# Performance work log

Measured on AMD Instinct MI355X. Metric: run time of the kernel, lower is better.

## Reference

```python
import jax, jax.numpy as jnp
import numpy as np

B, N, C, H = 4, 4096, 128, 4


def setup_inputs() -> dict:
    key = jax.random.key(0)
    ks = jax.random.split(key, 12)
    def rn(k, shape, s=0.02):
        return jax.random.normal(k, shape, jnp.float32) * s
    return dict(
        x=jax.random.normal(ks[0], (B, N, C), jnp.float32),
        p=jax.random.normal(ks[1], (B, N, 3), jnp.float32),
        fcl1_w=rn(ks[2], (C, C)), fcl1_b=jnp.zeros((C,), jnp.float32),
        # per-head (stacked over leading H axis) TransformerLayer params
        hq_w=rn(ks[3], (H, C, C)), hq_b=jnp.zeros((H, C), jnp.float32),
        hk_w=rn(ks[4], (H, C, C)), hk_b=jnp.zeros((H, C), jnp.float32),
        hv_w=rn(ks[5], (H, C, C)), hv_b=jnp.zeros((H, C), jnp.float32),
        pe1_w=rn(ks[6], (H, C, 3)), pe1_b=jnp.zeros((H, C), jnp.float32),  # Conv1d(3->C, k=1)
        pe2_w=rn(ks[7], (H, C, C)), pe2_b=jnp.zeros((H, C), jnp.float32),  # Conv1d(C->C, k=1)
        mh_w=rn(ks[8], (C, 4 * C)), mh_b=jnp.zeros((C,), jnp.float32),
        fcl2_w=rn(ks[9], (C, C)), fcl2_b=jnp.zeros((C,), jnp.float32),
    )


def reference(x, p, fcl1_w, fcl1_b, hq_w, hq_b, hk_w, hk_b, hv_w, hv_b,
              pe1_w, pe1_b, pe2_w, pe2_b, mh_w, mh_b, fcl2_w, fcl2_b):
    residual = x
    xf = x @ fcl1_w.T + fcl1_b  # fcl1
    scale = 1.0 / jnp.sqrt(jnp.asarray(C, jnp.float32))

    def head(qw, qb, kw, kb, vw, vb, p1w, p1b, p2w, p2b):
        # kernel-size-1 Conv1d == pointwise linear over coords
        pe = jax.nn.relu(jnp.einsum('bnd,cd->bnc', p, p1w) + p1b)
        pe = jnp.einsum('bnc,dc->bnd', pe, p2w) + p2b
        xh = xf + pe
        q = xh @ kw.T + kb  # note: original uses self.key for x_query
        k = xh @ qw.T + qb  # and self.query for x_key (name swap, kept faithful)
        v = xh @ vw.T + vb
        s = jax.nn.softmax(jnp.einsum('bnc,bmc->bnm', q, k) * scale, axis=-1)
        return jnp.einsum('bnm,bmc->bnc', s, v)

    outs = jax.vmap(head)(hq_w, hq_b, hk_w, hk_b, hv_w, hv_b,
                          pe1_w, pe1_b, pe2_w, pe2_b)  # [H,B,N,C]
    cat = jnp.moveaxis(outs, 0, 2).reshape(B, N, H * C)  # concat head1..head4 on last dim
    y = cat @ mh_w.T + mh_b
    y = y @ fcl2_w.T + fcl2_b
    mu = jnp.mean(y, axis=-1, keepdims=True)
    var = jnp.var(y, axis=-1, keepdims=True)
    y = (y - mu) / jnp.sqrt(var + 1e-5)  # torch.layer_norm, no affine
    return (y + residual, p)
```

## Files before the change

kernel.cpp:

```cpp
#include <hip/hip_runtime.h>
#include <hip/hip_bf16.h>

typedef __bf16 bf16;
typedef bf16 bf16x8 __attribute__((ext_vector_type(8)));
typedef float f32x4 __attribute__((ext_vector_type(4)));

static __device__ __forceinline__ f32x4 mfma16(bf16x8 a, bf16x8 b, f32x4 c) {
  return __builtin_amdgcn_mfma_f32_16x16x32_bf16(a, b, c, 0, 0, 0);
}

typedef __attribute__((address_space(3))) void lds_t;
typedef const __attribute__((address_space(1))) void gm_t;

#define N_SEG 18
#define TOTAL_CONV 2511616

__global__ void probe_k(const unsigned short* __restrict__ xr, int* __restrict__ flag) {
  int wild = 0;
#pragma unroll
  for (int i = 0; i < 8; i++) {
    unsigned short w = xr[threadIdx.x * 8 + i];
    int e = (w >> 7) & 0xFF;
    if (e < 110 || e > 134) wild++;
  }
#pragma unroll
  for (int off = 1; off < 64; off <<= 1) wild += __shfl_xor(wild, off);
  if (threadIdx.x == 0) *flag = (wild > 64) ? 1 : 0;
}

struct ConvArgs { const void* src[N_SEG]; };

__global__ __launch_bounds__(256) void convall_k(ConvArgs a, bf16* __restrict__ dst,
                                                 void* __restrict__ outp,
                                                 const int* __restrict__ flag) {
  const int ends[N_SEG] = {2097152, 2146304, 2162688, 2162816, 2228352, 2228864,
                           2294400, 2294912, 2360448, 2360960, 2362496, 2363008,
                           2428544, 2429056, 2494592, 2495104, 2511488, 2511616};
  int i = blockIdx.x * 256 + threadIdx.x;
  if (i >= TOTAL_CONV) {
    int j = i - TOTAL_CONV;
    if (j < 49152) {
      if (*flag) ((float*)outp)[2097152 + j] = ((const float*)a.src[1])[j];
      else       ((bf16*)outp)[2097152 + j]  = ((const bf16*)a.src[1])[j];
    }
    return;
  }
  int s = 0;
  while (i >= ends[s]) s++;
  int j = i - (s ? ends[s - 1] : 0);
  if (*flag) dst[i] = (bf16)((const float*)a.src[s])[j];
  else       dst[i] = ((const bf16*)a.src[s])[j];
}

__global__ __launch_bounds__(256, 2) void pre_k(
    const bf16* __restrict__ x, const bf16* __restrict__ p,
    const bf16* __restrict__ f1w, const bf16* __restrict__ f1b,
    const bf16* __restrict__ pe1w, const bf16* __restrict__ pe1b,
    const bf16* __restrict__ pe2w, const bf16* __restrict__ pe2b,
    const bf16* __restrict__ Wq, const bf16* __restrict__ Bq,
    const bf16* __restrict__ Wk, const bf16* __restrict__ Bk,
    const bf16* __restrict__ Wv, const bf16* __restrict__ Bv,
    bf16* __restrict__ qo, bf16* __restrict__ ko, bf16* __restrict__ vo)
{
  const int lane = threadIdx.x & 63;
  const int wave = threadIdx.x >> 6;
  const int quad = lane >> 4;
  const int n15 = lane & 15;
  const int h = blockIdx.y;
  const int r0 = blockIdx.x * 64;
  const int wr = wave * 16;

  __shared__ bf16 tile[9216];

  f32x4 acc[8];
  const f32x4 zz = {};

  {
    bf16x8 ap = {};
    if (quad == 0) {
      const bf16* pr = p + (long)(r0 + wr + n15) * 3;
      ap[0] = pr[0]; ap[1] = pr[1]; ap[2] = pr[2];
    }
#pragma unroll
    for (int ct = 0; ct < 8; ct++) {
      bf16x8 bw = {};
      if (quad == 0) {
        const bf16* wp = pe1w + ((long)h * 128 + ct * 16 + n15) * 3;
        bw[0] = wp[0]; bw[1] = wp[1]; bw[2] = wp[2];
      }
      acc[ct] = mfma16(ap, bw, zz);
    }
#pragma unroll
    for (int ct = 0; ct < 8; ct++) {
      const int col = ct * 16 + n15;
      const float bb = (float)pe1b[h * 128 + col];
#pragma unroll
      for (int r = 0; r < 4; r++)
        tile[(wr + quad * 4 + r) * 136 + col] = (bf16)fmaxf(acc[ct][r] + bb, 0.f);
    }
  }

#pragma unroll
  for (int ct = 0; ct < 8; ct++) acc[ct] = zz;
#pragma unroll
  for (int kk = 0; kk < 4; kk++) {
    const int ka = kk * 32 + quad * 8;
    bf16x8 a0 = *(const bf16x8*)&tile[(wr + n15) * 136 + ka];
#pragma unroll
    for (int ct = 0; ct < 8; ct++) {
      bf16x8 wf = *(const bf16x8*)(pe2w + (long)h * 16384 + (long)(ct * 16 + n15) * 128 + ka);
      acc[ct] = mfma16(a0, wf, acc[ct]);
    }
  }
#pragma unroll
  for (int kk = 0; kk < 4; kk++) {
    const int ka = kk * 32 + quad * 8;
    bf16x8 a0 = *(const bf16x8*)(x + (long)(r0 + wr + n15) * 128 + ka);
#pragma unroll
    for (int ct = 0; ct < 8; ct++) {
      bf16x8 wf = *(const bf16x8*)(f1w + (long)(ct * 16 + n15) * 128 + ka);
      acc[ct] = mfma16(a0, wf, acc[ct]);
    }
  }
#pragma unroll
  for (int ct = 0; ct < 8; ct++) {
    const int col = ct * 16 + n15;
    const float bv = (float)pe2b[h * 128 + col] + (float)f1b[col];
#pragma unroll
    for (int r = 0; r < 4; r++)
      tile[(wr + quad * 4 + r) * 136 + col] = (bf16)(acc[ct][r] + bv);
  }

  bf16x8 af[4];
#pragma unroll
  for (int kk = 0; kk < 4; kk++)
    af[kk] = *(const bf16x8*)&tile[(wr + n15) * 136 + kk * 32 + quad * 8];

#pragma unroll
  for (int m = 0; m < 2; m++) {
    f32x4 a2[8];
#pragma unroll
    for (int ct = 0; ct < 8; ct++) a2[ct] = zz;
    const bf16* Wm = (m == 0) ? Wq : Wk;
#pragma unroll
    for (int kk = 0; kk < 4; kk++) {
      const int ka = kk * 32 + quad * 8;
#pragma unroll
      for (int ct = 0; ct < 8; ct++) {
        bf16x8 wf = *(const bf16x8*)(Wm + (long)h * 16384 + (long)(ct * 16 + n15) * 128 + ka);
        a2[ct] = mfma16(af[kk], wf, a2[ct]);
      }
    }
    bf16* oz = ((m == 0) ? qo : ko) + (long)h * 2097152;
    const bf16* Bz = (m == 0) ? Bq : Bk;
    const float sc = (m == 0) ? 0.12751743f : 1.0f;
#pragma unroll
    for (int ct = 0; ct < 8; ct++) {
      const int col = ct * 16 + n15;
      const float bv = (float)Bz[h * 128 + col];
#pragma unroll
      for (int r = 0; r < 4; r++)
        oz[(long)(r0 + wr + quad * 4 + r) * 128 + col] = (bf16)((a2[ct][r] + bv) * sc);
    }
  }

  {
    f32x4 a2[8];
#pragma unroll
    for (int ct = 0; ct < 8; ct++) a2[ct] = zz;
#pragma unroll
    for (int kk = 0; kk < 4; kk++) {
      const int ka = kk * 32 + quad * 8;
#pragma unroll
      for (int ct = 0; ct < 8; ct++) {
        bf16x8 wf = *(const bf16x8*)(Wv + (long)h * 16384 + (long)(ct * 16 + n15) * 128 + ka);
        a2[ct] = mfma16(af[kk], wf, a2[ct]);
      }
    }
    __syncthreads();
#pragma unroll
    for (int ct = 0; ct < 8; ct++) {
      const int col = ct * 16 + n15;
      const float bv = (float)Bv[h * 128 + col];
#pragma unroll
      for (int r = 0; r < 4; r++)
        tile[col * 72 + (wr + quad * 4 + r)] = (bf16)(a2[ct][r] + bv);
    }
    __syncthreads();
    bf16* vz = vo + (long)h * 2097152;
#pragma unroll
    for (int i = 0; i < 16; i++) {
      const int c = wave * 32 + i * 2 + (lane >> 5);
      const int m2 = (lane & 31) * 2;
      *(unsigned int*)&vz[(long)c * 16384 + r0 + m2] =
          *(const unsigned int*)&tile[c * 72 + m2];
    }
  }
}

__global__ __launch_bounds__(256, 2) void attn_k(
    const bf16* __restrict__ Q, const bf16* __restrict__ Kg,
    const bf16* __restrict__ vT, bf16* __restrict__ Op, float* __restrict__ ls)
{
  const int lane = threadIdx.x & 63;
  const int wave = threadIdx.x >> 6;
  const int quad = lane >> 4;
  const int n15 = lane & 15;
  const int qt = blockIdx.x >> 1;
  const int half = blockIdx.x & 1;
  const int b = blockIdx.y, h = blockIdx.z;
  const long qkBase = ((long)h * 4 + b) * 4096 * 128;
  const long vBase = (long)h * (128L * 16384) + (long)b * 4096;
  const int wrow = qt * 128 + wave * 32;
  const int kvStart = half * 2048;

  __shared__ bf16 Kt[2][64 * 128];
  __shared__ bf16 Vt[2][128 * 64];
  __shared__ bf16 Pt[8][1024];

  bf16x8 qf[2][4];
#pragma unroll
  for (int g = 0; g < 2; g++)
#pragma unroll
    for (int kk = 0; kk < 4; kk++)
      qf[g][kk] = *(const bf16x8*)(Q + qkBase + (long)(wrow + g * 16 + n15) * 128 + kk * 32 + quad * 8);

  const int krl  = lane >> 4;
  const int kpch = lane & 15;
  const int vcl  = lane >> 3;
  const int vpch = lane & 7;

  f32x4 Om[2][8] = {};
  float l_part[2][4] = {};

#pragma unroll
  for (int i = 0; i < 4; i++) {
    const int row = wave * 16 + i * 4 + krl;
    const int ch = kpch ^ (row & 15);
    __builtin_amdgcn_global_load_lds(
        (gm_t*)(Kg + qkBase + (long)(kvStart + row) * 128 + ch * 8),
        (lds_t*)&Kt[0][(wave * 16 + i * 4) * 128], 16, 0, 0);
  }
#pragma unroll
  for (int i = 0; i < 4; i++) {
    const int c = wave * 32 + i * 8 + vcl;
    const int vch = vpch ^ (c & 7);
    __builtin_amdgcn_global_load_lds(
        (gm_t*)(vT + vBase + (long)c * 16384 + kvStart + vch * 8),
        (lds_t*)&Vt[0][(wave * 32 + i * 8) * 64], 16, 0, 0);
  }

  for (int it = 0; it < 32; it++) {
    __syncthreads();
    const int cb = it & 1;
    if (it + 1 < 32) {
      const int kv1 = kvStart + (it + 1) * 64;
      const int nb = cb ^ 1;
#pragma unroll
      for (int i = 0; i < 4; i++) {
        const int row = wave * 16 + i * 4 + krl;
        const int ch = kpch ^ (row & 15);
        __builtin_amdgcn_global_load_lds(
            (gm_t*)(Kg + qkBase + (long)(kv1 + row) * 128 + ch * 8),
            (lds_t*)&Kt[nb][(wave * 16 + i * 4) * 128], 16, 0, 0);
      }
#pragma unroll
      for (int i = 0; i < 4; i++) {
        const int c = wave * 32 + i * 8 + vcl;
        const int vch = vpch ^ (c & 7);
        __builtin_amdgcn_global_load_lds(
            (gm_t*)(vT + vBase + (long)c * 16384 + kv1 + vch * 8),
            (lds_t*)&Vt[nb][(wave * 32 + i * 8) * 64], 16, 0, 0);
      }
    }

    f32x4 S[2][4] = {};
#pragma unroll
    for (int kk = 0; kk < 4; kk++) {
#pragma unroll
      for (int ct = 0; ct < 4; ct++) {
        bf16x8 kf = *(const bf16x8*)&Kt[cb][(ct * 16 + n15) * 128 + (((kk * 4 + quad) ^ n15) * 8)];
        S[0][ct] = mfma16(qf[0][kk], kf, S[0][ct]);
        S[1][ct] = mfma16(qf[1][kk], kf, S[1][ct]);
      }
    }

#pragma unroll
    for (int g = 0; g < 2; g++)
#pragma unroll
      for (int ct = 0; ct < 4; ct++)
#pragma unroll
        for (int r = 0; r < 4; r++) {
          float e = __builtin_amdgcn_exp2f(S[g][ct][r]);
          l_part[g][r] += e;
          const int row = quad * 4 + r;
          const int kv = ct * 16 + n15;
          Pt[wave * 2 + g][row * 64 + ((((kv >> 3) ^ (row & 7)) * 8)) + (kv & 7)] = (bf16)e;
        }

#pragma unroll
    for (int kk = 0; kk < 2; kk++) {
      bf16x8 vf[8];
#pragma unroll
      for (int ct = 0; ct < 8; ct++) {
        const int c = ct * 16 + n15;
        vf[ct] = *(const bf16x8*)&Vt[cb][c * 64 + (((kk * 4 + quad) ^ (c & 7)) * 8)];
      }
#pragma unroll
      for (int g = 0; g < 2; g++) {
        bf16x8 pf = *(const bf16x8*)&Pt[wave * 2 + g][n15 * 64 + (((kk * 4 + quad) ^ (n15 & 7)) * 8)];
#pragma unroll
        for (int ct = 0; ct < 8; ct++)
          Om[g][ct] = mfma16(pf, vf[ct], Om[g][ct]);
      }
    }
  }

#pragma unroll
  for (int g = 0; g < 2; g++) {
#pragma unroll
    for (int r = 0; r < 4; r++) {
      float s = l_part[g][r];
#pragma unroll
      for (int off = 1; off < 16; off <<= 1) s += __shfl_xor(s, off);
      if (n15 == 0)
        ls[((long)half * 4 + h) * 16384 + b * 4096 + wrow + g * 16 + quad * 4 + r] = s;
    }
    const long ob = (long)half * 8388608 + (long)(b * 4096 + wrow + g * 16 + quad * 4) * 512 + h * 128;
#pragma unroll
    for (int ct = 0; ct < 8; ct++)
#pragma unroll
      for (int r = 0; r < 4; r++)
        Op[ob + (long)r * 512 + ct * 16 + n15] = (bf16)Om[g][ct][r];
  }
}

__global__ __launch_bounds__(256) void tail_k(
    const bf16* __restrict__ Op, const float* __restrict__ ls,
    const bf16* __restrict__ mhw, const bf16* __restrict__ mhb,
    const bf16* __restrict__ f2w, const bf16* __restrict__ f2b,
    const void* __restrict__ xraw, void* __restrict__ outraw,
    const int* __restrict__ flag)
{
  const int lane = threadIdx.x & 63;
  const int wave = threadIdx.x >> 6;
  const int quad = lane >> 4;
  const int n15 = lane & 15;
  const int r0 = blockIdx.x * 64 + wave * 16;
  __shared__ bf16 y1t[64][136];

  float invA[4];
#pragma unroll
  for (int hh = 0; hh < 4; hh++) {
    const float l0 = ls[(long)hh * 16384 + r0 + n15];
    const float l1 = ls[(long)(4 + hh) * 16384 + r0 + n15];
    invA[hh] = 1.f / (l0 + l1);
  }

  f32x4 acc[8] = {};
  for (int k0 = 0; k0 < 512; k0 += 32) {
    const int hh = k0 >> 7;
    const int ka = k0 + quad * 8;
    bf16x8 v0 = *(const bf16x8*)(Op + (long)(r0 + n15) * 512 + ka);
    bf16x8 v1 = *(const bf16x8*)(Op + 8388608L + (long)(r0 + n15) * 512 + ka);
    bf16x8 a0;
#pragma unroll
    for (int j = 0; j < 8; j++)
      a0[j] = (bf16)(((float)v0[j] + (float)v1[j]) * invA[hh]);
#pragma unroll
    for (int ct = 0; ct < 8; ct++) {
      bf16x8 wf = *(const bf16x8*)(mhw + (long)(ct * 16 + n15) * 512 + ka);
      acc[ct] = mfma16(a0, wf, acc[ct]);
    }
  }
#pragma unroll
  for (int ct = 0; ct < 8; ct++) {
    const float bv = (float)mhb[ct * 16 + n15];
#pragma unroll
    for (int r = 0; r < 4; r++)
      y1t[wave * 16 + quad * 4 + r][ct * 16 + n15] = (bf16)(acc[ct][r] + bv);
  }

  f32x4 acc2[8] = {};
  for (int k0 = 0; k0 < 128; k0 += 32) {
    const int ka = k0 + quad * 8;
    bf16x8 a0 = *(const bf16x8*)&y1t[wave * 16 + n15][ka];
#pragma unroll
    for (int ct = 0; ct < 8; ct++) {
      bf16x8 wf = *(const bf16x8*)(f2w + (long)(ct * 16 + n15) * 128 + ka);
      acc2[ct] = mfma16(a0, wf, acc2[ct]);
    }
  }

  float s1[4] = {}, s2[4] = {};
#pragma unroll
  for (int ct = 0; ct < 8; ct++) {
    const float bv = (float)f2b[ct * 16 + n15];
#pragma unroll
    for (int r = 0; r < 4; r++) {
      const float v = acc2[ct][r] + bv;
      acc2[ct][r] = v;
      s1[r] += v;
      s2[r] += v * v;
    }
  }
  float mu[4], inv[4];
#pragma unroll
  for (int r = 0; r < 4; r++) {
    float a = s1[r], b2 = s2[r];
#pragma unroll
    for (int off = 1; off < 16; off <<= 1) {
      a += __shfl_xor(a, off);
      b2 += __shfl_xor(b2, off);
    }
    mu[r] = a * (1.f / 128.f);
    const float var = fmaxf(b2 * (1.f / 128.f) - mu[r] * mu[r], 0.f);
    inv[r] = rsqrtf(var + 1e-5f);
  }

  const int isF32 = *flag;
#pragma unroll
  for (int ct = 0; ct < 8; ct++)
#pragma unroll
    for (int r = 0; r < 4; r++) {
      const long idx = (long)(r0 + quad * 4 + r) * 128 + ct * 16 + n15;
      const float resid = isF32 ? ((const float*)xraw)[idx]
                                : (float)((const bf16*)xraw)[idx];
      const float v = (acc2[ct][r] - mu[r]) * inv[r] + resid;
      if (isF32) ((float*)outraw)[idx] = v;
      else       ((bf16*)outraw)[idx] = (bf16)v;
    }
}

extern "C" void kernel_launch(void* const* d_in, const int* in_sizes, int n_in,
                              void* d_out, int out_size, void* d_ws, size_t ws_size,
                              hipStream_t stream)
{
  bf16* ws  = (bf16*)d_ws;
  bf16* q   = ws;
  bf16* kb  = ws + 8388608;
  bf16* vt  = ws + 16777216;
  bf16* Op  = ws + 25165824;
  float* lsb = (float*)(ws + 41943040);
  const long AR = 42205184;
  int* flag = (int*)(ws + 44720000);

  static const int counts[N_SEG] = {2097152, 49152, 16384, 128, 65536, 512, 65536, 512,
                                    65536, 512, 1536, 512, 65536, 512, 65536, 512, 16384, 128};
  long offs[N_SEG]; long o = AR;
  for (int i = 0; i < N_SEG; i++) { offs[i] = o; o += counts[i]; }
  bf16* xc    = ws + offs[0];
  bf16* pc    = ws + offs[1];
  bf16* f1w   = ws + offs[2];
  bf16* f1b   = ws + offs[3];
  bf16* hqw   = ws + offs[4];
  bf16* hqb   = ws + offs[5];
  bf16* hkw   = ws + offs[6];
  bf16* hkb   = ws + offs[7];
  bf16* hvw   = ws + offs[8];
  bf16* hvb   = ws + offs[9];
  bf16* pe1w  = ws + offs[10];
  bf16* pe1b  = ws + offs[11];
  bf16* pe2w  = ws + offs[12];
  bf16* pe2b  = ws + offs[13];
  bf16* mhw   = ws + offs[14];
  bf16* mhb   = ws + offs[15];
  bf16* f2w   = ws + offs[16];
  bf16* f2b   = ws + offs[17];

  probe_k<<<dim3(1), dim3(64), 0, stream>>>((const unsigned short*)d_in[0], flag);
  ConvArgs ca;
  for (int i = 0; i < N_SEG; i++) ca.src[i] = d_in[i];
  convall_k<<<dim3((TOTAL_CONV + 49152 + 255) / 256), dim3(256), 0, stream>>>(ca, ws + AR, d_out, flag);

  dim3 blk(256);
  pre_k<<<dim3(256, 4), blk, 0, stream>>>(xc, pc, f1w, f1b, pe1w, pe1b, pe2w, pe2b,
                                          hkw, hkb, hqw, hqb, hvw, hvb, q, kb, vt);
  attn_k<<<dim3(64, 4, 4), blk, 0, stream>>>(q, kb, vt, Op, lsb);
  tail_k<<<dim3(256), blk, 0, stream>>>(Op, lsb, mhw, mhb, f2w, f2b, d_in[0], d_out, flag);
}
```

Before: 360.8 us.

## Drop KV split in attention, normalize in-kernel, fold dtype probe into conversion

The attention kernel no longer splits the key/value range into two halves. Each block now processes all 4096 keys and normalizes by the row sum before writing a single bf16 concat buffer. This removes the partial-output and row-sum buffers and the combine step in the tail kernel, at the cost of half as many attention blocks (512 instead of 1024) with twice the loop length. The separate dtype-probe launch is also merged into the conversion kernel: every block now recomputes the flag from the first 512 elements of x, which removes one launch.

```diff
diff --git a/kernel.cpp b/kernel.cpp
--- a/kernel.cpp
+++ b/kernel.cpp
@@ -15,32 +15,35 @@
 #define N_SEG 18
 #define TOTAL_CONV 2511616
 
-__global__ void probe_k(const unsigned short* __restrict__ xr, int* __restrict__ flag) {
-  int wild = 0;
-#pragma unroll
-  for (int i = 0; i < 8; i++) {
-    unsigned short w = xr[threadIdx.x * 8 + i];
-    int e = (w >> 7) & 0xFF;
-    if (e < 110 || e > 134) wild++;
-  }
-#pragma unroll
-  for (int off = 1; off < 64; off <<= 1) wild += __shfl_xor(wild, off);
-  if (threadIdx.x == 0) *flag = (wild > 64) ? 1 : 0;
-}
-
 struct ConvArgs { const void* src[N_SEG]; };
 
 __global__ __launch_bounds__(256) void convall_k(ConvArgs a, bf16* __restrict__ dst,
                                                  void* __restrict__ outp,
-                                                 const int* __restrict__ flag) {
+                                                 int* __restrict__ flag) {
   const int ends[N_SEG] = {2097152, 2146304, 2162688, 2162816, 2228352, 2228864,
                            2294400, 2294912, 2360448, 2360960, 2362496, 2363008,
                            2428544, 2429056, 2494592, 2495104, 2511488, 2511616};
+  const unsigned short* xr = (const unsigned short*)a.src[0];
+  int wild = 0;
+#pragma unroll
+  for (int j = 0; j < 2; j++) {
+    unsigned short w = xr[threadIdx.x * 2 + j];
+    int e = (w >> 7) & 0xFF;
+    if (e < 110 || e > 134) wild++;
+  }
+#pragma unroll
+  for (int off = 1; off < 64; off <<= 1) wild += __shfl_xor(wild, off);
+  __shared__ int red[4];
+  if ((threadIdx.x & 63) == 0) red[threadIdx.x >> 6] = wild;
+  __syncthreads();
+  const int isF32 = (red[0] + red[1] + red[2] + red[3]) > 64;
+  if (blockIdx.x == 0 && threadIdx.x == 0) *flag = isF32;
+
   int i = blockIdx.x * 256 + threadIdx.x;
   if (i >= TOTAL_CONV) {
     int j = i - TOTAL_CONV;
     if (j < 49152) {
-      if (*flag) ((float*)outp)[2097152 + j] = ((const float*)a.src[1])[j];
+      if (isF32) ((float*)outp)[2097152 + j] = ((const float*)a.src[1])[j];
       else       ((bf16*)outp)[2097152 + j]  = ((const bf16*)a.src[1])[j];
     }
     return;
@@ -48,7 +51,7 @@
   int s = 0;
   while (i >= ends[s]) s++;
   int j = i - (s ? ends[s - 1] : 0);
-  if (*flag) dst[i] = (bf16)((const float*)a.src[s])[j];
+  if (isF32) dst[i] = (bf16)((const float*)a.src[s])[j];
   else       dst[i] = ((const bf16*)a.src[s])[j];
 }
 
@@ -200,19 +203,16 @@
 
 __global__ __launch_bounds__(256, 2) void attn_k(
     const bf16* __restrict__ Q, const bf16* __restrict__ Kg,
-    const bf16* __restrict__ vT, bf16* __restrict__ Op, float* __restrict__ ls)
+    const bf16* __restrict__ vT, bf16* __restrict__ cat)
 {
   const int lane = threadIdx.x & 63;
   const int wave = threadIdx.x >> 6;
   const int quad = lane >> 4;
   const int n15 = lane & 15;
-  const int qt = blockIdx.x >> 1;
-  const int half = blockIdx.x & 1;
   const int b = blockIdx.y, h = blockIdx.z;
   const long qkBase = ((long)h * 4 + b) * 4096 * 128;
   const long vBase = (long)h * (128L * 16384) + (long)b * 4096;
-  const int wrow = qt * 128 + wave * 32;
-  const int kvStart = half * 2048;
+  const int wrow = blockIdx.x * 128 + wave * 32;
 
   __shared__ bf16 Kt[2][64 * 128];
   __shared__ bf16 Vt[2][128 * 64];
@@ -238,7 +238,7 @@
     const int row = wave * 16 + i * 4 + krl;
     const int ch = kpch ^ (row & 15);
     __builtin_amdgcn_global_load_lds(
-        (gm_t*)(Kg + qkBase + (long)(kvStart + row) * 128 + ch * 8),
+        (gm_t*)(Kg + qkBase + (long)row * 128 + ch * 8),
         (lds_t*)&Kt[0][(wave * 16 + i * 4) * 128], 16, 0, 0);
   }
 #pragma unroll
@@ -246,15 +246,15 @@
     const int c = wave * 32 + i * 8 + vcl;
     const int vch = vpch ^ (c & 7);
     __builtin_amdgcn_global_load_lds(
-        (gm_t*)(vT + vBase + (long)c * 16384 + kvStart + vch * 8),
+        (gm_t*)(vT + vBase + (long)c * 16384 + vch * 8),
         (lds_t*)&Vt[0][(wave * 32 + i * 8) * 64], 16, 0, 0);
   }
 
-  for (int it = 0; it < 32; it++) {
+  for (int it = 0; it < 64; it++) {
     __syncthreads();
     const int cb = it & 1;
-    if (it + 1 < 32) {
-      const int kv1 = kvStart + (it + 1) * 64;
+    if (it + 1 < 64) {
+      const int kv1 = (it + 1) * 64;
       const int nb = cb ^ 1;
 #pragma unroll
       for (int i = 0; i < 4; i++) {
@@ -318,25 +318,25 @@
 
 #pragma unroll
   for (int g = 0; g < 2; g++) {
+    float inv[4];
 #pragma unroll
     for (int r = 0; r < 4; r++) {
       float s = l_part[g][r];
 #pragma unroll
       for (int off = 1; off < 16; off <<= 1) s += __shfl_xor(s, off);
-      if (n15 == 0)
-        ls[((long)half * 4 + h) * 16384 + b * 4096 + wrow + g * 16 + quad * 4 + r] = s;
-    }
-    const long ob = (long)half * 8388608 + (long)(b * 4096 + wrow + g * 16 + quad * 4) * 512 + h * 128;
+      inv[r] = 1.f / s;
+    }
+    const long ob = ((long)b * 4096 + wrow + g * 16 + quad * 4) * 512 + h * 128;
 #pragma unroll
     for (int ct = 0; ct < 8; ct++)
 #pragma unroll
       for (int r = 0; r < 4; r++)
-        Op[ob + (long)r * 512 + ct * 16 + n15] = (bf16)Om[g][ct][r];
+        cat[ob + (long)r * 512 + ct * 16 + n15] = (bf16)(Om[g][ct][r] * inv[r]);
   }
 }
 
 __global__ __launch_bounds__(256) void tail_k(
-    const bf16* __restrict__ Op, const float* __restrict__ ls,
+    const bf16* __restrict__ cat,
     const bf16* __restrict__ mhw, const bf16* __restrict__ mhb,
     const bf16* __restrict__ f2w, const bf16* __restrict__ f2b,
     const void* __restrict__ xraw, void* __restrict__ outraw,
@@ -349,24 +349,10 @@
   const int r0 = blockIdx.x * 64 + wave * 16;
   __shared__ bf16 y1t[64][136];
 
-  float invA[4];
-#pragma unroll
-  for (int hh = 0; hh < 4; hh++) {
-    const float l0 = ls[(long)hh * 16384 + r0 + n15];
-    const float l1 = ls[(long)(4 + hh) * 16384 + r0 + n15];
-    invA[hh] = 1.f / (l0 + l1);
-  }
-
   f32x4 acc[8] = {};
   for (int k0 = 0; k0 < 512; k0 += 32) {
-    const int hh = k0 >> 7;
     const int ka = k0 + quad * 8;
-    bf16x8 v0 = *(const bf16x8*)(Op + (long)(r0 + n15) * 512 + ka);
-    bf16x8 v1 = *(const bf16x8*)(Op + 8388608L + (long)(r0 + n15) * 512 + ka);
-    bf16x8 a0;
-#pragma unroll
-    for (int j = 0; j < 8; j++)
-      a0[j] = (bf16)(((float)v0[j] + (float)v1[j]) * invA[hh]);
+    bf16x8 a0 = *(const bf16x8*)(cat + (long)(r0 + n15) * 512 + ka);
 #pragma unroll
     for (int ct = 0; ct < 8; ct++) {
       bf16x8 wf = *(const bf16x8*)(mhw + (long)(ct * 16 + n15) * 512 + ka);
@@ -440,10 +426,9 @@
   bf16* q   = ws;
   bf16* kb  = ws + 8388608;
   bf16* vt  = ws + 16777216;
-  bf16* Op  = ws + 25165824;
-  float* lsb = (float*)(ws + 41943040);
-  const long AR = 42205184;
-  int* flag = (int*)(ws + 44720000);
+  bf16* cat = ws + 25165824;
+  const long AR = 33554432;
+  int* flag = (int*)(ws + 36066048);
 
   static const int counts[N_SEG] = {2097152, 49152, 16384, 128, 65536, 512, 65536, 512,
                                     65536, 512, 1536, 512, 65536, 512, 65536, 512, 16384, 128};
@@ -468,7 +453,6 @@
   bf16* f2w   = ws + offs[16];
   bf16* f2b   = ws + offs[17];
 
-  probe_k<<<dim3(1), dim3(64), 0, stream>>>((const unsigned short*)d_in[0], flag);
   ConvArgs ca;
   for (int i = 0; i < N_SEG; i++) ca.src[i] = d_in[i];
   convall_k<<<dim3((TOTAL_CONV + 49152 + 255) / 256), dim3(256), 0, stream>>>(ca, ws + AR, d_out, flag);
@@ -476,6 +460,6 @@
   dim3 blk(256);
   pre_k<<<dim3(256, 4), blk, 0, stream>>>(xc, pc, f1w, f1b, pe1w, pe1b, pe2w, pe2b,
                                           hkw, hkb, hqw, hqb, hvw, hvb, q, kb, vt);
-  attn_k<<<dim3(64, 4, 4), blk, 0, stream>>>(q, kb, vt, Op, lsb);
-  tail_k<<<dim3(256), blk, 0, stream>>>(Op, lsb, mhw, mhb, f2w, f2b, d_in[0], d_out, flag);
-}
+  attn_k<<<dim3(32, 4, 4), blk, 0, stream>>>(q, kb, vt, cat);
+  tail_k<<<dim3(256), blk, 0, stream>>>(cat, mhw, mhb, f2w, f2b, d_in[0], d_out, flag);
+}
```

Measured after the change: 358.2 us. No clear change (-0.7%).
